# Kernel tuning notes

Measured on AMD Instinct MI355X. Metric: run time of the kernel, lower is better.

The kernel has to match this reference:

```python
import jax, jax.numpy as jnp
import numpy as np

B, S, H, L, MAXS = 64, 512, 768, 32, 8


def setup_inputs() -> dict:
    key = jax.random.key(0)
    ks = jax.random.split(key, 10)
    def n(k, shape, s=1.0):
        return jax.random.normal(k, shape, dtype=jnp.float32) * s
    return {
        "tokens_rep": n(ks[0], (B, S, H)),
        "seq_rep": n(ks[1], (B, H)),
        "W_start": n(ks[2], (H,), 0.02), "b_start": n(ks[3], (1,), 0.02),
        "W_end": n(ks[4], (H,), 0.02), "b_end": n(ks[5], (1,), 0.02),
        "W_nspans": n(ks[6], (H, MAXS + 1), 0.02), "b_nspans": n(ks[7], (MAXS + 1,), 0.02),
        "W_span": n(ks[8], (H, L), 0.02), "b_span": n(ks[9], (L,), 0.02),
    }


def _forward(tokens_rep, seq_rep, W_start, b_start, W_end, b_end,
             W_nspans, b_nspans, W_span, b_span):
    Bd, Sd, Hd = tokens_rep.shape
    Ld = b_span.shape[0]
    K = b_nspans.shape[0] - 1  # max_spans

    # classifier heads (dropout = identity in eval)
    full_seq_logits = seq_rep @ W_span + b_span                      # [B,L]
    start_logits = jnp.einsum('bsh,h->bs', tokens_rep, W_start) + b_start  # [B,S]
    end_logits = jnp.einsum('bsh,h->bs', tokens_rep, W_end) + b_end        # [B,S]
    n_spans_logits = seq_rep @ W_nspans + b_nspans                   # [B,K+1]
    all_n_spans = jnp.argmax(n_spans_logits, axis=1).astype(jnp.int32)

    # prefix sums over seq for O(1) mean-pooling of arbitrary spans: P[:,e]-P[:,s]
    P = jnp.concatenate(
        [jnp.zeros((Bd, 1, Hd), tokens_rep.dtype), jnp.cumsum(tokens_rep, axis=1)], axis=1)

    def per_sample(full_row, starts, ends, Prow, n_spans):
        # top-k start/end positions; only the first n_spans of the sorted top-K matter.
        _, i_s = jax.lax.top_k(jax.nn.sigmoid(starts), K)
        _, i_e = jax.lax.top_k(jax.nn.sigmoid(ends), K)
        rank = jnp.arange(K, dtype=jnp.int32)
        ss = jnp.sort(jnp.where(rank < n_spans, i_s.astype(jnp.int32), Sd))
        es = jnp.sort(jnp.where(rank < n_spans, i_e.astype(jnp.int32), Sd))

        # greedy non-overlapping merge (faithful to get_top_spans_nongreedy)
        def cond(st):
            s_i, e_i, n_rem, last_end, cnt, sa, ea = st
            return (n_rem > 0) & (s_i < n_spans) & (e_i < n_spans)

        def body(st):
            s_i, e_i, n_rem, last_end, cnt, sa, ea = st
            s = ss[s_i]
            e = es[e_i]
            take = (e > s) & (s >= last_end)
            sa = sa.at[cnt].set(jnp.where(take, s, sa[cnt]))
            ea = ea.at[cnt].set(jnp.where(take, e, ea[cnt]))
            e_le_s = e <= s
            one = jnp.int32(1)
            zero = jnp.int32(0)
            s_i = s_i + jnp.where(take | ~e_le_s, one, zero)
            e_i = e_i + jnp.where(take | e_le_s, one, zero)
            last_end = jnp.where(take, e, last_end)
            t = take.astype(jnp.int32)
            return (s_i, e_i, n_rem - t, last_end, cnt + t, sa, ea)

        z = jnp.int32(0)
        init = (z, z, n_spans, z, z,
                jnp.zeros((K,), jnp.int32), jnp.zeros((K,), jnp.int32))
        *_, cnt, sa, ea = jax.lax.while_loop(cond, body, init)

        valid = rank < cnt
        vf = valid.astype(full_row.dtype)
        lens = jnp.maximum(ea - sa, 1).astype(full_row.dtype)
        vecs = (Prow[ea] - Prow[sa]) / lens[:, None]       # [K,H] span means
        logits = vecs @ W_span + b_span                    # [K,L]
        neg = jnp.finfo(logits.dtype).min
        masked = jnp.where(valid[:, None], logits, neg)
        spans_multi = jnp.where(cnt > 0, jnp.max(masked, axis=0), jnp.zeros((), full_row.dtype))
        span_labels = jnp.argmax(masked, axis=1)
        labels_multi = jnp.zeros((Ld,), full_row.dtype).at[span_labels].max(vf)
        starts_multi = jnp.zeros((Sd,), full_row.dtype).at[sa].max(vf)
        ends_multi = jnp.zeros((Sd,), full_row.dtype).at[ea].max(vf)

        labels_single = jax.nn.one_hot(jnp.argmax(full_row), Ld, dtype=full_row.dtype)
        starts_single = jax.nn.one_hot(jnp.argmax(starts), Sd, dtype=full_row.dtype)
        ends_single = jax.nn.one_hot(jnp.argmax(ends), Sd, dtype=full_row.dtype)

        multi = n_spans > 1
        spans = jnp.where(multi, spans_multi, full_row)
        labels = jnp.where(multi, labels_multi, labels_single)
        s_oh = jnp.where(multi, starts_multi, starts_single)
        e_oh = jnp.where(multi, ends_multi, ends_single)
        return spans, labels, s_oh, e_oh

    spans, labels, s_oh, e_oh = jax.vmap(per_sample)(
        full_seq_logits, start_logits, end_logits, P, all_n_spans)
    # (start_logits, end_logits, label_logits, n_spans_logits, preds_starts, preds_ends, preds_labels)
    return start_logits, end_logits, spans, n_spans_logits, s_oh, e_oh, labels


def reference(tokens_rep, seq_rep, W_start, b_start, W_end, b_end,
              W_nspans, b_nspans, W_span, b_span):
    return _forward(tokens_rep, seq_rep, W_start, b_start, W_end, b_end,
                    W_nspans, b_nspans, W_span, b_span)
```

## Files before the change

### kernel.cpp

```cpp
#include <hip/hip_runtime.h>
#include <float.h>

#define NB 64
#define NS 512
#define NH 768
#define NL 32
#define NK 8

#define OFF_START 0
#define OFF_END   (NB*NS)
#define OFF_SPANS (2*NB*NS)
#define OFF_NSP   (2*NB*NS + NB*NL)
#define OFF_SOH   (2*NB*NS + NB*NL + NB*9)
#define OFF_EOH   (3*NB*NS + NB*NL + NB*9)
#define OFF_LAB   (4*NB*NS + NB*NL + NB*9)

__global__ __launch_bounds__(256) void kA(const float* __restrict__ T,
                                          const float* __restrict__ Ws,
                                          const float* __restrict__ We,
                                          const float* __restrict__ bs,
                                          const float* __restrict__ be,
                                          float* __restrict__ out) {
    int row  = blockIdx.x * 4 + (threadIdx.x >> 6);
    int lane = threadIdx.x & 63;
    const float4* p   = (const float4*)(T + (size_t)row * NH);
    const float4* w4s = (const float4*)Ws;
    const float4* w4e = (const float4*)We;
    float accs = 0.f, acce = 0.f;
#pragma unroll
    for (int c = 0; c < 3; ++c) {
        float4 t = p[lane + c * 64];
        float4 a = w4s[lane + c * 64];
        float4 b = w4e[lane + c * 64];
        accs += t.x * a.x + t.y * a.y + t.z * a.z + t.w * a.w;
        acce += t.x * b.x + t.y * b.y + t.z * b.z + t.w * b.w;
    }
#pragma unroll
    for (int off = 32; off > 0; off >>= 1) {
        accs += __shfl_down(accs, off);
        acce += __shfl_down(acce, off);
    }
    if (lane == 0) {
        out[OFF_START + row] = accs + bs[0];
        out[OFF_END   + row] = acce + be[0];
    }
}

__device__ __forceinline__ void waveTop8(const float* __restrict__ g, int lane,
                                         int* __restrict__ dst) {
    float v0 = g[lane],       v1 = g[lane + 64],  v2 = g[lane + 128], v3 = g[lane + 192];
    float v4 = g[lane + 256], v5 = g[lane + 320], v6 = g[lane + 384], v7 = g[lane + 448];
#pragma unroll
    for (int r = 0; r < 8; ++r) {
        float bv = v0; int bi = lane;
        if (v1 > bv) { bv = v1; bi = lane + 64; }
        if (v2 > bv) { bv = v2; bi = lane + 128; }
        if (v3 > bv) { bv = v3; bi = lane + 192; }
        if (v4 > bv) { bv = v4; bi = lane + 256; }
        if (v5 > bv) { bv = v5; bi = lane + 320; }
        if (v6 > bv) { bv = v6; bi = lane + 384; }
        if (v7 > bv) { bv = v7; bi = lane + 448; }
#pragma unroll
        for (int off = 32; off > 0; off >>= 1) {
            float ov = __shfl_xor(bv, off);
            int   oi = __shfl_xor(bi, off);
            if (ov > bv || (ov == bv && oi < bi)) { bv = ov; bi = oi; }
        }
        if (lane == 0) dst[r] = bi;
        if      (bi == lane)       v0 = -FLT_MAX;
        else if (bi == lane + 64)  v1 = -FLT_MAX;
        else if (bi == lane + 128) v2 = -FLT_MAX;
        else if (bi == lane + 192) v3 = -FLT_MAX;
        else if (bi == lane + 256) v4 = -FLT_MAX;
        else if (bi == lane + 320) v5 = -FLT_MAX;
        else if (bi == lane + 384) v6 = -FLT_MAX;
        else if (bi == lane + 448) v7 = -FLT_MAX;
    }
}

__global__ __launch_bounds__(512) void kBC(const float* __restrict__ T,
                                           const float* __restrict__ seq_rep,
                                           const float* __restrict__ W_nspans,
                                           const float* __restrict__ b_nspans,
                                           const float* __restrict__ W_span,
                                           const float* __restrict__ b_span,
                                           float* __restrict__ out,
                                           int* __restrict__ wsI,
                                           float* __restrict__ wsF,
                                           float* __restrict__ wsLG) {
    int k = blockIdx.x, b = blockIdx.y;
    int tid = threadIdx.x, wave = tid >> 6, lane = tid & 63;

    __shared__ int    topS[NK], topE[NK];
    __shared__ float  part[6][41];
    __shared__ float  fl[NL], nsp[9];
    __shared__ int    saS[NK], eaS[NK];
    __shared__ int    meta[3];
    __shared__ float4 sm4[8][192];
    __shared__ float  vec[NH];
    __shared__ float  pl[8][32];

    if (tid < 64) {
        waveTop8(out + OFF_START + b * NS, tid, topS);
    } else if (tid < 128) {
        waveTop8(out + OFF_END + b * NS, tid - 64, topE);
    } else if (tid < 128 + 246) {
        int t = tid - 128, g = t / 41, l = t % 41;
        int h0 = g * 128;
        const float* sr = seq_rep + b * NH;
        float acc = 0.f;
        if (l < 32) {
            for (int h = h0; h < h0 + 128; ++h) acc += sr[h] * W_span[h * NL + l];
        } else {
            int j = l - 32;
            for (int h = h0; h < h0 + 128; ++h) acc += sr[h] * W_nspans[h * 9 + j];
        }
        part[g][l] = acc;
    }
    __syncthreads();
    if (tid < 41) {
        float a = 0.f;
#pragma unroll
        for (int g = 0; g < 6; ++g) a += part[g][tid];
        if (tid < 32) fl[tid] = a + b_span[tid];
        else          nsp[tid - 32] = a + b_nspans[tid - 32];
    }
    __syncthreads();

    if (tid == 0) {
        int ns = 0; float bv = nsp[0];
        for (int j = 1; j < 9; ++j) if (nsp[j] > bv) { bv = nsp[j]; ns = j; }

        int ss[NK], es[NK];
        for (int i = 0; i < NK; ++i) {
            ss[i] = (i < ns) ? topS[i] : NS;
            es[i] = (i < ns) ? topE[i] : NS;
        }
        for (int i = 1; i < NK; ++i) {
            int v = ss[i], j = i - 1;
            while (j >= 0 && ss[j] > v) { ss[j + 1] = ss[j]; --j; }
            ss[j + 1] = v;
        }
        for (int i = 1; i < NK; ++i) {
            int v = es[i], j = i - 1;
            while (j >= 0 && es[j] > v) { es[j + 1] = es[j]; --j; }
            es[j + 1] = v;
        }
        int sa[NK], ea[NK];
        for (int i = 0; i < NK; ++i) { sa[i] = 0; ea[i] = 0; }
        int si = 0, ei = 0, nrem = ns, last = 0, cnt = 0;
        while (nrem > 0 && si < ns && ei < ns) {
            int s = ss[si], e = es[ei];
            bool take = (e > s) && (s >= last);
            if (take) { sa[cnt] = s; ea[cnt] = e; last = e; ++cnt; --nrem; }
            if (e > s) ++si;
            if (take || e <= s) ++ei;
        }
        int af = 0; float fv = fl[0];
        for (int l = 1; l < NL; ++l) if (fl[l] > fv) { fv = fl[l]; af = l; }

        meta[0] = ns; meta[1] = cnt; meta[2] = af;
        for (int i = 0; i < NK; ++i) { saS[i] = sa[i]; eaS[i] = ea[i]; }
    }
    __syncthreads();

    int ns = meta[0], cnt = meta[1];

    if (k == NK) {
        if (tid < 9)  out[OFF_NSP + b * 9 + tid] = nsp[tid];
        if (tid < 32) wsF[b * 32 + tid] = fl[tid];
        if (tid == 0) {
            int* W = wsI + b * 32;
            W[0] = ns; W[1] = cnt; W[2] = meta[2]; W[3] = topS[0]; W[4] = topE[0];
            for (int i = 0; i < NK; ++i) { W[5 + i] = saS[i]; W[13 + i] = eaS[i]; }
        }
        return;
    }

    if (ns <= 1 || k >= cnt) return;

    int s = saS[k], e = eaS[k];
    float4 a0 = make_float4(0.f, 0.f, 0.f, 0.f), a1 = a0, a2 = a0;
    const float4* Tb = (const float4*)(T + (size_t)b * NS * NH);
    int r = s + wave;
    for (; r + 8 < e; r += 16) {
        const float4* p = Tb + (size_t)r * 192 + lane;
        const float4* q = Tb + (size_t)(r + 8) * 192 + lane;
        float4 x0 = p[0], x1 = p[64], x2 = p[128];
        float4 y0 = q[0], y1 = q[64], y2 = q[128];
        a0.x += x0.x + y0.x; a0.y += x0.y + y0.y; a0.z += x0.z + y0.z; a0.w += x0.w + y0.w;
        a1.x += x1.x + y1.x; a1.y += x1.y + y1.y; a1.z += x1.z + y1.z; a1.w += x1.w + y1.w;
        a2.x += x2.x + y2.x; a2.y += x2.y + y2.y; a2.z += x2.z + y2.z; a2.w += x2.w + y2.w;
    }
    if (r < e) {
        const float4* p = Tb + (size_t)r * 192 + lane;
        float4 x0 = p[0], x1 = p[64], x2 = p[128];
        a0.x += x0.x; a0.y += x0.y; a0.z += x0.z; a0.w += x0.w;
        a1.x += x1.x; a1.y += x1.y; a1.z += x1.z; a1.w += x1.w;
        a2.x += x2.x; a2.y += x2.y; a2.z += x2.z; a2.w += x2.w;
    }
    sm4[wave][lane]       = a0;
    sm4[wave][lane + 64]  = a1;
    sm4[wave][lane + 128] = a2;
    __syncthreads();

    if (tid < 192) {
        float inv = 1.f / (float)(e - s);
        float4 v = make_float4(0.f, 0.f, 0.f, 0.f);
#pragma unroll
        for (int w = 0; w < 8; ++w) {
            float4 u = sm4[w][tid];
            v.x += u.x; v.y += u.y; v.z += u.z; v.w += u.w;
        }
        v.x *= inv; v.y *= inv; v.z *= inv; v.w *= inv;
        ((float4*)vec)[tid] = v;
    }
    __syncthreads();

    if (tid < 256) {
        int g = tid >> 5, l = tid & 31;
        float acc = 0.f;
        int h0 = g * 96;
        for (int h = h0; h < h0 + 96; ++h) acc += vec[h] * W_span[h * NL + l];
        pl[g][l] = acc;
    }
    __syncthreads();
    if (tid < 32) {
        float a = b_span[tid];
#pragma unroll
        for (int gg = 0; gg < 8; ++gg) a += pl[gg][tid];
        wsLG[(b * NK + k) * NL + tid] = a;
    }
}

__global__ __launch_bounds__(512) void kD(const int* __restrict__ wsI,
                                          const float* __restrict__ wsF,
                                          const float* __restrict__ wsLG,
                                          float* __restrict__ out) {
    int b = blockIdx.x, t = threadIdx.x;
    const int* W = wsI + b * 32;
    int ns = W[0], cnt = W[1], af = W[2], as_ = W[3], ae_ = W[4];
    bool multi = ns > 1;
    __shared__ int   sa[NK], ea[NK], sl[NK];
    __shared__ float lgs[NK][NL];
    if (t < NK) { sa[t] = W[5 + t]; ea[t] = W[13 + t]; }
    __syncthreads();
    if (t < NK) {
        if (multi && t < cnt) {
            const float* Lp = wsLG + (b * NK + t) * NL;
            float bv = Lp[0]; int bi = 0;
            for (int l = 0; l < NL; ++l) {
                lgs[t][l] = Lp[l];
                if (Lp[l] > bv) { bv = Lp[l]; bi = l; }
            }
            sl[t] = bi;
        } else sl[t] = -1;
    }
    __syncthreads();
    if (t < NL) {
        float sp, lb;
        if (multi) {
            float mx = 0.f;
            if (cnt > 0) {
                mx = -FLT_MAX;
                for (int k = 0; k < cnt; ++k) mx = fmaxf(mx, lgs[k][t]);
            }
            sp = mx;
            lb = 0.f;
            for (int k = 0; k < cnt; ++k) if (sl[k] == t) lb = 1.f;
        } else {
            sp = wsF[b * NL + t];
            lb = (t == af) ? 1.f : 0.f;
        }
        out[OFF_SPANS + b * NL + t] = sp;
        out[OFF_LAB   + b * NL + t] = lb;
    }
    {
        float svv = 0.f, evv = 0.f;
        if (multi) {
            for (int k = 0; k < cnt; ++k) {
                if (sa[k] == t) svv = 1.f;
                if (ea[k] == t) evv = 1.f;
            }
        } else {
            svv = (t == as_) ? 1.f : 0.f;
            evv = (t == ae_) ? 1.f : 0.f;
        }
        out[OFF_SOH + b * NS + t] = svv;
        out[OFF_EOH + b * NS + t] = evv;
    }
}

extern "C" void kernel_launch(void* const* d_in, const int* in_sizes, int n_in,
                              void* d_out, int out_size, void* d_ws, size_t ws_size,
                              hipStream_t stream) {
    const float* tokens   = (const float*)d_in[0];
    const float* seq_rep  = (const float*)d_in[1];
    const float* W_start  = (const float*)d_in[2];
    const float* b_start  = (const float*)d_in[3];
    const float* W_end    = (const float*)d_in[4];
    const float* b_end    = (const float*)d_in[5];
    const float* W_nspans = (const float*)d_in[6];
    const float* b_nspans = (const float*)d_in[7];
    const float* W_span   = (const float*)d_in[8];
    const float* b_span   = (const float*)d_in[9];
    float* out = (float*)d_out;

    int*   wsI  = (int*)d_ws;
    float* wsF  = (float*)((char*)d_ws + NB * 32 * sizeof(int));
    float* wsLG = (float*)((char*)d_ws + NB * 32 * sizeof(int) + NB * NL * sizeof(float));

    kA<<<(NB * NS) / 4, 256, 0, stream>>>(tokens, W_start, W_end, b_start, b_end, out);
    kBC<<<dim3(NK + 1, NB), 512, 0, stream>>>(tokens, seq_rep, W_nspans, b_nspans,
                                              W_span, b_span, out, wsI, wsF, wsLG);
    kD<<<NB, 512, 0, stream>>>(wsI, wsF, wsLG, out);
}
```

Measured before the change: 50.45 us.

## Precompute 8-row chunk sums in score kernel to shorten span mean-pooling reads

The start/end score kernel now also sums each group of 8 token rows through shared memory and writes these chunk sums to workspace. The span pooling in kBC then reads whole chunks from that workspace and reads raw token rows only for the partial edges of each span. This cuts the re-reads of the large token tensor for long spans, at the cost of an extra write of about 12.5 MB and a block barrier in kA.

```diff
diff --git a/kernel.cpp b/kernel.cpp
--- a/kernel.cpp
+++ b/kernel.cpp
@@ -6,6 +6,7 @@
 #define NH 768
 #define NL 32
 #define NK 8
+#define NCH 64
 
 #define OFF_START 0
 #define OFF_END   (NB*NS)
@@ -15,23 +16,30 @@
 #define OFF_EOH   (3*NB*NS + NB*NL + NB*9)
 #define OFF_LAB   (4*NB*NS + NB*NL + NB*9)
 
-__global__ __launch_bounds__(256) void kA(const float* __restrict__ T,
+__global__ __launch_bounds__(512) void kA(const float* __restrict__ T,
                                           const float* __restrict__ Ws,
                                           const float* __restrict__ We,
                                           const float* __restrict__ bs,
                                           const float* __restrict__ be,
-                                          float* __restrict__ out) {
-    int row  = blockIdx.x * 4 + (threadIdx.x >> 6);
-    int lane = threadIdx.x & 63;
+                                          float* __restrict__ out,
+                                          float4* __restrict__ wsC) {
+    int j    = blockIdx.x;
+    int wave = threadIdx.x >> 6, lane = threadIdx.x & 63;
+    int row  = j * 8 + wave;
+
+    __shared__ float4 smc[8][192];
+
     const float4* p   = (const float4*)(T + (size_t)row * NH);
     const float4* w4s = (const float4*)Ws;
     const float4* w4e = (const float4*)We;
     float accs = 0.f, acce = 0.f;
+    float4 x[3];
 #pragma unroll
     for (int c = 0; c < 3; ++c) {
         float4 t = p[lane + c * 64];
         float4 a = w4s[lane + c * 64];
         float4 b = w4e[lane + c * 64];
+        x[c] = t;
         accs += t.x * a.x + t.y * a.y + t.z * a.z + t.w * a.w;
         acce += t.x * b.x + t.y * b.y + t.z * b.z + t.w * b.w;
     }
@@ -43,6 +51,20 @@
     if (lane == 0) {
         out[OFF_START + row] = accs + bs[0];
         out[OFF_END   + row] = acce + be[0];
+    }
+
+    smc[wave][lane]       = x[0];
+    smc[wave][lane + 64]  = x[1];
+    smc[wave][lane + 128] = x[2];
+    __syncthreads();
+    if (threadIdx.x < 192) {
+        float4 v = make_float4(0.f, 0.f, 0.f, 0.f);
+#pragma unroll
+        for (int w = 0; w < 8; ++w) {
+            float4 u = smc[w][threadIdx.x];
+            v.x += u.x; v.y += u.y; v.z += u.z; v.w += u.w;
+        }
+        wsC[(size_t)j * 192 + threadIdx.x] = v;
     }
 }
 
@@ -78,7 +100,16 @@
     }
 }
 
+#define ACC3(P) do { \
+    const float4* _p = (P); \
+    float4 _x0 = _p[0], _x1 = _p[64], _x2 = _p[128]; \
+    a0.x += _x0.x; a0.y += _x0.y; a0.z += _x0.z; a0.w += _x0.w; \
+    a1.x += _x1.x; a1.y += _x1.y; a1.z += _x1.z; a1.w += _x1.w; \
+    a2.x += _x2.x; a2.y += _x2.y; a2.z += _x2.z; a2.w += _x2.w; \
+} while (0)
+
 __global__ __launch_bounds__(512) void kBC(const float* __restrict__ T,
+                                           const float4* __restrict__ wsC,
                                            const float* __restrict__ seq_rep,
                                            const float* __restrict__ W_nspans,
                                            const float* __restrict__ b_nspans,
@@ -182,23 +213,22 @@
     int s = saS[k], e = eaS[k];
     float4 a0 = make_float4(0.f, 0.f, 0.f, 0.f), a1 = a0, a2 = a0;
     const float4* Tb = (const float4*)(T + (size_t)b * NS * NH);
-    int r = s + wave;
-    for (; r + 8 < e; r += 16) {
-        const float4* p = Tb + (size_t)r * 192 + lane;
-        const float4* q = Tb + (size_t)(r + 8) * 192 + lane;
-        float4 x0 = p[0], x1 = p[64], x2 = p[128];
-        float4 y0 = q[0], y1 = q[64], y2 = q[128];
-        a0.x += x0.x + y0.x; a0.y += x0.y + y0.y; a0.z += x0.z + y0.z; a0.w += x0.w + y0.w;
-        a1.x += x1.x + y1.x; a1.y += x1.y + y1.y; a1.z += x1.z + y1.z; a1.w += x1.w + y1.w;
-        a2.x += x2.x + y2.x; a2.y += x2.y + y2.y; a2.z += x2.z + y2.z; a2.w += x2.w + y2.w;
-    }
-    if (r < e) {
-        const float4* p = Tb + (size_t)r * 192 + lane;
-        float4 x0 = p[0], x1 = p[64], x2 = p[128];
-        a0.x += x0.x; a0.y += x0.y; a0.z += x0.z; a0.w += x0.w;
-        a1.x += x1.x; a1.y += x1.y; a1.z += x1.z; a1.w += x1.w;
-        a2.x += x2.x; a2.y += x2.y; a2.z += x2.z; a2.w += x2.w;
-    }
+    const float4* Cb = wsC + (size_t)b * NCH * 192;
+
+    int c0 = (s + 7) >> 3, c1 = e >> 3;
+    if (c0 < c1) {
+        int c = c0 + wave;
+        for (; c + 8 < c1; c += 16) {
+            ACC3(Cb + (size_t)c * 192 + lane);
+            ACC3(Cb + (size_t)(c + 8) * 192 + lane);
+        }
+        if (c < c1) ACC3(Cb + (size_t)c * 192 + lane);
+        for (int r = s + wave; r < (c0 << 3); r += 8) ACC3(Tb + (size_t)r * 192 + lane);
+        for (int r = (c1 << 3) + wave; r < e; r += 8) ACC3(Tb + (size_t)r * 192 + lane);
+    } else {
+        for (int r = s + wave; r < e; r += 8) ACC3(Tb + (size_t)r * 192 + lane);
+    }
+
     sm4[wave][lane]       = a0;
     sm4[wave][lane + 64]  = a1;
     sm4[wave][lane + 128] = a2;
@@ -306,12 +336,15 @@
     const float* b_span   = (const float*)d_in[9];
     float* out = (float*)d_out;
 
-    int*   wsI  = (int*)d_ws;
-    float* wsF  = (float*)((char*)d_ws + NB * 32 * sizeof(int));
-    float* wsLG = (float*)((char*)d_ws + NB * 32 * sizeof(int) + NB * NL * sizeof(float));
-
-    kA<<<(NB * NS) / 4, 256, 0, stream>>>(tokens, W_start, W_end, b_start, b_end, out);
-    kBC<<<dim3(NK + 1, NB), 512, 0, stream>>>(tokens, seq_rep, W_nspans, b_nspans,
+    size_t wsCbytes = (size_t)NB * NCH * NH * sizeof(float);
+    float4* wsC = (float4*)d_ws;
+    int*    wsI = (int*)((char*)d_ws + wsCbytes);
+    float*  wsF = (float*)((char*)d_ws + wsCbytes + NB * 32 * sizeof(int));
+    float*  wsLG = (float*)((char*)d_ws + wsCbytes + NB * 32 * sizeof(int)
+                            + NB * NL * sizeof(float));
+
+    kA<<<(NB * NS) / 8, 512, 0, stream>>>(tokens, W_start, W_end, b_start, b_end, out, wsC);
+    kBC<<<dim3(NK + 1, NB), 512, 0, stream>>>(tokens, wsC, seq_rep, W_nspans, b_nspans,
                                               W_span, b_span, out, wsI, wsF, wsLG);
     kD<<<NB, 512, 0, stream>>>(wsI, wsF, wsLG, out);
 }
```

After: 44.06 us. 12.7% less time.
